# Optimization experiments

Measured on AMD Instinct MI355X. Metric: run time of the kernel, lower is better.

The kernel has to match this reference:

```python
import jax, jax.numpy as jnp
import numpy as np

B, C, T = 32, 1536, 2048
BN = 128  # bottleneck channels


def setup_inputs() -> dict:
    key = jax.random.key(0)
    k1, k2, k3, k4, k5, k6 = jax.random.split(key, 6)
    x = jax.random.normal(k1, (B, C, T), dtype=jnp.float32)
    padding_mask = jax.random.randint(k2, (B, T), 0, 2) == 1
    W_tdnn = jax.random.normal(k3, (BN, C), dtype=jnp.float32) * (1.0 / np.sqrt(C))
    b_tdnn = jax.random.normal(k4, (BN,), dtype=jnp.float32) * 0.01
    W_attn = jax.random.normal(k5, (C, BN), dtype=jnp.float32) * (1.0 / np.sqrt(BN))
    b_attn = jax.random.normal(k6, (C,), dtype=jnp.float32) * 0.01
    return {"x": x, "padding_mask": padding_mask, "W_tdnn": W_tdnn,
            "b_tdnn": b_tdnn, "W_attn": W_attn, "b_attn": b_attn}


def reference(x, padding_mask, W_tdnn, b_tdnn, W_attn, b_attn):
    # pointwise conv1 (k=1) == channel-wise matmul: (B,C,T) -> (B,BN,T)
    e = jnp.tanh(jnp.einsum('oc,bct->bot', W_tdnn, x) + b_tdnn[None, :, None])
    # pointwise conv2: (B,BN,T) -> (B,C,T)
    a = jnp.einsum('co,bot->bct', W_attn, e) + b_attn[None, :, None]
    a = jnp.where(padding_mask[:, None, :], -1e9, a)
    alpha = jax.nn.softmax(a, axis=2)  # (B,C,T)
    mean = jnp.sum(alpha * x, axis=2)  # (B,C)
    var = jnp.sum(alpha * (x - mean[:, :, None]) ** 2, axis=2)
    std = jnp.sqrt(jnp.clip(var, 1e-9, None))
    return jnp.concatenate([mean, std], axis=1)  # (B,2C)
```

## Files before the change

kernel.cpp:

```cpp
#include <hip/hip_runtime.h>
#include <math.h>

#define Bn  32
#define Cn  1536
#define Tn  2048
#define BNn 128
#define SHIFT 12.0f

typedef __attribute__((ext_vector_type(8))) short bf16x8;
typedef __attribute__((ext_vector_type(4))) float fx4;

__device__ __forceinline__ unsigned int f2bf1(float f) {
    unsigned int u = __float_as_uint(f);
    return (u + 0x7fffu + ((u >> 16) & 1u)) >> 16;
}
__device__ __forceinline__ float fast_tanh(float v) {
    return 1.f - 2.f / (__expf(2.f * v) + 1.f);
}

__global__ void k_prep(const float* __restrict__ W1f, const float* __restrict__ Waf,
                       short* __restrict__ W1b, short* __restrict__ Wab) {
    int i = blockIdx.x * 256 + threadIdx.x;
    if (i < BNn * Cn) {
        W1b[i] = (short)f2bf1(W1f[i]);
        Wab[i] = (short)f2bf1(Waf[i]);
    }
}

__global__ __launch_bounds__(256, 3) void k_fused(
    const float* __restrict__ x, const short* __restrict__ W1,
    const float* __restrict__ bias, const short* __restrict__ Wab,
    const int* __restrict__ mask, float* __restrict__ part)
{
    __shared__ short sA[128 * 64];
    __shared__ short sE[128 * 128];

    const int b    = blockIdx.y;
    const int t0g  = blockIdx.x * 128;
    const int tid  = threadIdx.x;
    const int lane = tid & 63;
    const int wv   = tid >> 6;
    const int ln   = lane & 15;
    const int g    = lane >> 4;
    const int wt   = (wv & 1) * 64;
    const int wo   = (wv >> 1) * 64;

    const float* xb = x + (size_t)b * Cn * Tn;
    const float* xt = xb + t0g;

    const int t4 = (tid & 31) * 4;
    const int cq = (tid >> 5) * 4;

    fx4 acc[4][4];
    #pragma unroll
    for (int i = 0; i < 4; ++i)
        #pragma unroll
        for (int j = 0; j < 4; ++j) acc[i][j] = (fx4){0.f, 0.f, 0.f, 0.f};

    for (int k0 = 0; k0 < Cn; k0 += 64) {
        float4 xr[2][4];
        #pragma unroll
        for (int p = 0; p < 2; ++p) {
            const int c = cq + p * 32;
            #pragma unroll
            for (int j = 0; j < 4; ++j)
                xr[p][j] = *(const float4*)(xt + (size_t)(k0 + c + j) * Tn + t4);
        }
        __syncthreads();
        #pragma unroll
        for (int p = 0; p < 2; ++p) {
            const int c   = cq + p * 32;
            const int blk = c >> 3;
            const int sub = c & 7;
            #pragma unroll
            for (int i = 0; i < 4; ++i) {
                const int t = t4 + i;
                unsigned int lo = f2bf1(((const float*)&xr[p][0])[i]) |
                                  (f2bf1(((const float*)&xr[p][1])[i]) << 16);
                unsigned int hi = f2bf1(((const float*)&xr[p][2])[i]) |
                                  (f2bf1(((const float*)&xr[p][3])[i]) << 16);
                const int idx = t * 64 + ((blk ^ (t & 7)) << 3) + sub;
                *(uint2*)(sA + idx) = make_uint2(lo, hi);
            }
        }
        __syncthreads();

        #pragma unroll
        for (int kt = 0; kt < 2; ++kt) {
            bf16x8 bq[4];
            #pragma unroll
            for (int nn = 0; nn < 4; ++nn)
                bq[nn] = *(const bf16x8*)(W1 + (size_t)(wo + nn * 16 + ln) * Cn
                                          + k0 + kt * 32 + g * 8);
            bf16x8 af[4];
            #pragma unroll
            for (int mm = 0; mm < 4; ++mm) {
                const int t = wt + mm * 16 + ln;
                af[mm] = *(const bf16x8*)(sA + t * 64 + (((kt * 4 + g) ^ (t & 7)) << 3));
            }
            #pragma unroll
            for (int mm = 0; mm < 4; ++mm)
                #pragma unroll
                for (int nn = 0; nn < 4; ++nn)
                    acc[mm][nn] = __builtin_amdgcn_mfma_f32_16x16x32_bf16(
                        af[mm], bq[nn], acc[mm][nn], 0, 0, 0);
        }
    }

    float bs[4];
    #pragma unroll
    for (int nn = 0; nn < 4; ++nn) bs[nn] = bias[wo + nn * 16 + ln];

    #pragma unroll
    for (int mm = 0; mm < 4; ++mm)
        #pragma unroll
        for (int nn = 0; nn < 4; ++nn) {
            #pragma unroll
            for (int r = 0; r < 4; ++r) {
                const int t = wt + mm * 16 + g * 4 + r;
                const int o = wo + nn * 16 + ln;
                const float v = fast_tanh(acc[mm][nn][r] + bs[nn]);
                sE[t * 128 + (((o >> 3) ^ (t & 15)) << 3) + (o & 7)] = (short)f2bf1(v);
            }
        }
    __syncthreads();

    bf16x8 af2[4][4];
    #pragma unroll
    for (int mt = 0; mt < 4; ++mt)
        #pragma unroll
        for (int kt = 0; kt < 4; ++kt) {
            const int t = wt + mt * 16 + ln;
            af2[mt][kt] = *(const bf16x8*)(sE + t * 128 + (((kt * 4 + g) ^ (t & 15)) << 3));
        }

    int4 mv[4];
    #pragma unroll
    for (int mt = 0; mt < 4; ++mt)
        mv[mt] = *(const int4*)(mask + (size_t)b * Tn + t0g + wt + mt * 16 + g * 4);

    const int wc    = (wv >> 1) * 32;
    const int chunk = blockIdx.x * 2 + (wv & 1);

    for (int cc = 0; cc < Cn; cc += 64) {
        const int c0 = (Cn - 64) - cc;
        #pragma unroll
        for (int nt = 0; nt < 2; ++nt) {
            const int cr = c0 + wc + nt * 16 + ln;

            bf16x8 bfr[4];
            #pragma unroll
            for (int kt = 0; kt < 4; ++kt)
                bfr[kt] = *(const bf16x8*)(Wab + (size_t)cr * BNn + kt * 32 + g * 8);

            float4 xq[4];
            #pragma unroll
            for (int mt = 0; mt < 4; ++mt)
                xq[mt] = *(const float4*)(xb + (size_t)cr * Tn
                                          + t0g + wt + mt * 16 + g * 4);

            fx4 a2[4];
            #pragma unroll
            for (int mt = 0; mt < 4; ++mt) a2[mt] = (fx4){0.f, 0.f, 0.f, 0.f};

            #pragma unroll
            for (int kt = 0; kt < 4; ++kt)
                #pragma unroll
                for (int mt = 0; mt < 4; ++mt)
                    a2[mt] = __builtin_amdgcn_mfma_f32_16x16x32_bf16(
                        af2[mt][kt], bfr[kt], a2[mt], 0, 0, 0);

            float s0 = 0.f, s1 = 0.f, s2 = 0.f;
            #pragma unroll
            for (int mt = 0; mt < 4; ++mt) {
                #pragma unroll
                for (int r = 0; r < 4; ++r) {
                    const int msk = ((const int*)&mv[mt])[r];
                    const float p = msk ? 0.f : __expf(a2[mt][r] - SHIFT);
                    const float xv = ((const float*)&xq[mt])[r];
                    s0 += p;
                    s1 += p * xv;
                    s2 += p * xv * xv;
                }
            }
            s0 += __shfl_xor(s0, 16); s1 += __shfl_xor(s1, 16); s2 += __shfl_xor(s2, 16);
            s0 += __shfl_xor(s0, 32); s1 += __shfl_xor(s1, 32); s2 += __shfl_xor(s2, 32);
            if (g == 0) {
                *(float4*)&part[(((size_t)b * 32 + chunk) * Cn + cr) * 4] =
                    make_float4(s0, s1, s2, 0.f);
            }
        }
    }
}

__global__ void k_merge(const float* __restrict__ part, float* __restrict__ out) {
    const int i = blockIdx.x * 256 + threadIdx.x;
    if (i >= Bn * Cn) return;
    const int b = i / Cn, c = i - b * Cn;
    float s0 = 0.f, s1 = 0.f, s2 = 0.f;
    #pragma unroll 8
    for (int sp = 0; sp < 32; ++sp) {
        const float4 v = *(const float4*)&part[(((size_t)b * 32 + sp) * Cn + c) * 4];
        s0 += v.x; s1 += v.y; s2 += v.z;
    }
    const float mean = s1 / s0;
    const float var  = fmaxf(s2 / s0 - mean * mean, 1e-9f);
    out[(size_t)b * (2 * Cn) + c]      = mean;
    out[(size_t)b * (2 * Cn) + Cn + c] = sqrtf(var);
}

extern "C" void kernel_launch(void* const* d_in, const int* in_sizes, int n_in,
                              void* d_out, int out_size, void* d_ws, size_t ws_size,
                              hipStream_t stream) {
    const float* x      = (const float*)d_in[0];
    const int*   mask   = (const int*)d_in[1];
    const float* W_tdnn = (const float*)d_in[2];
    const float* b_tdnn = (const float*)d_in[3];
    const float* W_attn = (const float*)d_in[4];
    float* out = (float*)d_out;

    short* W1b  = (short*)d_ws;
    short* Wab  = W1b + (size_t)BNn * Cn;
    float* part = (float*)(Wab + (size_t)BNn * Cn);

    k_prep<<<dim3((BNn * Cn + 255) / 256), 256, 0, stream>>>(W_tdnn, W_attn, W1b, Wab);
    k_fused<<<dim3(Tn / 128, Bn), 256, 0, stream>>>(x, W1b, b_tdnn, Wab, mask, part);
    k_merge<<<dim3((Bn * Cn + 255) / 256), 256, 0, stream>>>(part, out);
}
```

Measured before the change: 632.6 us.

## Software-pipeline global loads in both GEMM phases with register double buffering

Both main loops now use explicit register double buffering. In phase 1, the next 64-channel slice of x is loaded into registers while MFMAs run on the current LDS tile. In phase 2, the next Wab and x fragments are prefetched before the current tile's MFMA, exp and reduction, hiding global load latency behind compute. The extra register buffers raise pressure, so launch bounds drop from 3 to 2 blocks per SM, which lowers occupancy in exchange for intra-wave overlap.

```diff
diff --git a/kernel.cpp b/kernel.cpp
--- a/kernel.cpp
+++ b/kernel.cpp
@@ -27,7 +27,91 @@
     }
 }
 
-__global__ __launch_bounds__(256, 3) void k_fused(
+
+#define P1_LOAD(XR, K0) do {                                                  \
+    _Pragma("unroll") for (int p = 0; p < 2; ++p) {                           \
+        const int c_ = cq + p * 32;                                           \
+        _Pragma("unroll") for (int j = 0; j < 4; ++j)                         \
+            XR[p][j] = *(const float4*)(xt + (size_t)((K0) + c_ + j) * Tn + t4); \
+    }                                                                         \
+} while (0)
+
+#define P1_WRITE(XR) do {                                                     \
+    _Pragma("unroll") for (int p = 0; p < 2; ++p) {                           \
+        const int c_   = cq + p * 32;                                         \
+        const int blk_ = c_ >> 3;                                             \
+        const int sub_ = c_ & 7;                                              \
+        _Pragma("unroll") for (int i2 = 0; i2 < 4; ++i2) {                    \
+            const int t_ = t4 + i2;                                           \
+            unsigned int lo_ = f2bf1(((const float*)&XR[p][0])[i2]) |         \
+                               (f2bf1(((const float*)&XR[p][1])[i2]) << 16);  \
+            unsigned int hi_ = f2bf1(((const float*)&XR[p][2])[i2]) |         \
+                               (f2bf1(((const float*)&XR[p][3])[i2]) << 16);  \
+            const int idx_ = t_ * 64 + ((blk_ ^ (t_ & 7)) << 3) + sub_;       \
+            *(uint2*)(sA + idx_) = make_uint2(lo_, hi_);                      \
+        }                                                                     \
+    }                                                                         \
+} while (0)
+
+#define P1_COMPUTE(K0) do {                                                   \
+    _Pragma("unroll") for (int kt = 0; kt < 2; ++kt) {                        \
+        bf16x8 bq_[4];                                                        \
+        _Pragma("unroll") for (int nn = 0; nn < 4; ++nn)                      \
+            bq_[nn] = *(const bf16x8*)(W1 + (size_t)(wo + nn * 16 + ln) * Cn  \
+                                       + (K0) + kt * 32 + g * 8);             \
+        bf16x8 af_[4];                                                        \
+        _Pragma("unroll") for (int mm = 0; mm < 4; ++mm) {                    \
+            const int t_ = wt + mm * 16 + ln;                                 \
+            af_[mm] = *(const bf16x8*)(sA + t_ * 64                           \
+                                       + (((kt * 4 + g) ^ (t_ & 7)) << 3));   \
+        }                                                                     \
+        _Pragma("unroll") for (int mm = 0; mm < 4; ++mm)                      \
+            _Pragma("unroll") for (int nn = 0; nn < 4; ++nn)                  \
+                acc[mm][nn] = __builtin_amdgcn_mfma_f32_16x16x32_bf16(        \
+                    af_[mm], bq_[nn], acc[mm][nn], 0, 0, 0);                  \
+    }                                                                         \
+} while (0)
+
+#define P2_CR(I) (((Cn - 64) - ((I) >> 1) * 64) + wc + ((I) & 1) * 16 + ln)
+
+#define P2_LOAD(BQ, XQ, I) do {                                               \
+    const int cr_ = P2_CR(I);                                                 \
+    _Pragma("unroll") for (int kt = 0; kt < 4; ++kt)                          \
+        BQ[kt] = *(const bf16x8*)(Wab + (size_t)cr_ * BNn + kt * 32 + g * 8); \
+    _Pragma("unroll") for (int mt = 0; mt < 4; ++mt)                          \
+        XQ[mt] = *(const float4*)(xb + (size_t)cr_ * Tn                       \
+                                  + t0g + wt + mt * 16 + g * 4);              \
+} while (0)
+
+#define P2_COMPUTE(BQ, XQ, I) do {                                           \
+    fx4 a2_[4];                                                               \
+    _Pragma("unroll") for (int mt = 0; mt < 4; ++mt)                          \
+        a2_[mt] = (fx4){0.f, 0.f, 0.f, 0.f};                                  \
+    _Pragma("unroll") for (int kt = 0; kt < 4; ++kt)                          \
+        _Pragma("unroll") for (int mt = 0; mt < 4; ++mt)                      \
+            a2_[mt] = __builtin_amdgcn_mfma_f32_16x16x32_bf16(                \
+                af2[mt][kt], BQ[kt], a2_[mt], 0, 0, 0);                       \
+    float s0_ = 0.f, s1_ = 0.f, s2_ = 0.f;                                    \
+    _Pragma("unroll") for (int mt = 0; mt < 4; ++mt) {                        \
+        _Pragma("unroll") for (int r = 0; r < 4; ++r) {                       \
+            const int msk_ = ((const int*)&mv[mt])[r];                        \
+            const float p_ = msk_ ? 0.f : __expf(a2_[mt][r] - SHIFT);         \
+            const float xv_ = ((const float*)&XQ[mt])[r];                     \
+            s0_ += p_; s1_ += p_ * xv_; s2_ += p_ * xv_ * xv_;                \
+        }                                                                     \
+    }                                                                         \
+    s0_ += __shfl_xor(s0_, 16); s1_ += __shfl_xor(s1_, 16);                   \
+    s2_ += __shfl_xor(s2_, 16);                                               \
+    s0_ += __shfl_xor(s0_, 32); s1_ += __shfl_xor(s1_, 32);                   \
+    s2_ += __shfl_xor(s2_, 32);                                               \
+    if (g == 0) {                                                             \
+        const int cr_ = P2_CR(I);                                             \
+        *(float4*)&part[(((size_t)b * 32 + chunk) * Cn + cr_) * 4] =          \
+            make_float4(s0_, s1_, s2_, 0.f);                                  \
+    }                                                                         \
+} while (0)
+
+__global__ __launch_bounds__(256, 2) void k_fused(
     const float* __restrict__ x, const short* __restrict__ W1,
     const float* __restrict__ bias, const short* __restrict__ Wab,
     const int* __restrict__ mask, float* __restrict__ part)
@@ -57,54 +141,19 @@
         #pragma unroll
         for (int j = 0; j < 4; ++j) acc[i][j] = (fx4){0.f, 0.f, 0.f, 0.f};
 
-    for (int k0 = 0; k0 < Cn; k0 += 64) {
-        float4 xr[2][4];
-        #pragma unroll
-        for (int p = 0; p < 2; ++p) {
-            const int c = cq + p * 32;
-            #pragma unroll
-            for (int j = 0; j < 4; ++j)
-                xr[p][j] = *(const float4*)(xt + (size_t)(k0 + c + j) * Tn + t4);
-        }
-        __syncthreads();
-        #pragma unroll
-        for (int p = 0; p < 2; ++p) {
-            const int c   = cq + p * 32;
-            const int blk = c >> 3;
-            const int sub = c & 7;
-            #pragma unroll
-            for (int i = 0; i < 4; ++i) {
-                const int t = t4 + i;
-                unsigned int lo = f2bf1(((const float*)&xr[p][0])[i]) |
-                                  (f2bf1(((const float*)&xr[p][1])[i]) << 16);
-                unsigned int hi = f2bf1(((const float*)&xr[p][2])[i]) |
-                                  (f2bf1(((const float*)&xr[p][3])[i]) << 16);
-                const int idx = t * 64 + ((blk ^ (t & 7)) << 3) + sub;
-                *(uint2*)(sA + idx) = make_uint2(lo, hi);
-            }
-        }
-        __syncthreads();
-
-        #pragma unroll
-        for (int kt = 0; kt < 2; ++kt) {
-            bf16x8 bq[4];
-            #pragma unroll
-            for (int nn = 0; nn < 4; ++nn)
-                bq[nn] = *(const bf16x8*)(W1 + (size_t)(wo + nn * 16 + ln) * Cn
-                                          + k0 + kt * 32 + g * 8);
-            bf16x8 af[4];
-            #pragma unroll
-            for (int mm = 0; mm < 4; ++mm) {
-                const int t = wt + mm * 16 + ln;
-                af[mm] = *(const bf16x8*)(sA + t * 64 + (((kt * 4 + g) ^ (t & 7)) << 3));
-            }
-            #pragma unroll
-            for (int mm = 0; mm < 4; ++mm)
-                #pragma unroll
-                for (int nn = 0; nn < 4; ++nn)
-                    acc[mm][nn] = __builtin_amdgcn_mfma_f32_16x16x32_bf16(
-                        af[mm], bq[nn], acc[mm][nn], 0, 0, 0);
-        }
+    float4 xrA[2][4], xrB[2][4];
+    P1_LOAD(xrA, 0);
+    for (int k0 = 0; k0 < Cn; k0 += 128) {
+        __syncthreads();
+        P1_WRITE(xrA);
+        __syncthreads();
+        P1_LOAD(xrB, k0 + 64);
+        P1_COMPUTE(k0);
+        __syncthreads();
+        P1_WRITE(xrB);
+        __syncthreads();
+        if (k0 + 128 < Cn) P1_LOAD(xrA, k0 + 128);
+        P1_COMPUTE(k0 + 64);
     }
 
     float bs[4];
@@ -142,54 +191,14 @@
     const int wc    = (wv >> 1) * 32;
     const int chunk = blockIdx.x * 2 + (wv & 1);
 
-    for (int cc = 0; cc < Cn; cc += 64) {
-        const int c0 = (Cn - 64) - cc;
-        #pragma unroll
-        for (int nt = 0; nt < 2; ++nt) {
-            const int cr = c0 + wc + nt * 16 + ln;
-
-            bf16x8 bfr[4];
-            #pragma unroll
-            for (int kt = 0; kt < 4; ++kt)
-                bfr[kt] = *(const bf16x8*)(Wab + (size_t)cr * BNn + kt * 32 + g * 8);
-
-            float4 xq[4];
-            #pragma unroll
-            for (int mt = 0; mt < 4; ++mt)
-                xq[mt] = *(const float4*)(xb + (size_t)cr * Tn
-                                          + t0g + wt + mt * 16 + g * 4);
-
-            fx4 a2[4];
-            #pragma unroll
-            for (int mt = 0; mt < 4; ++mt) a2[mt] = (fx4){0.f, 0.f, 0.f, 0.f};
-
-            #pragma unroll
-            for (int kt = 0; kt < 4; ++kt)
-                #pragma unroll
-                for (int mt = 0; mt < 4; ++mt)
-                    a2[mt] = __builtin_amdgcn_mfma_f32_16x16x32_bf16(
-                        af2[mt][kt], bfr[kt], a2[mt], 0, 0, 0);
-
-            float s0 = 0.f, s1 = 0.f, s2 = 0.f;
-            #pragma unroll
-            for (int mt = 0; mt < 4; ++mt) {
-                #pragma unroll
-                for (int r = 0; r < 4; ++r) {
-                    const int msk = ((const int*)&mv[mt])[r];
-                    const float p = msk ? 0.f : __expf(a2[mt][r] - SHIFT);
-                    const float xv = ((const float*)&xq[mt])[r];
-                    s0 += p;
-                    s1 += p * xv;
-                    s2 += p * xv * xv;
-                }
-            }
-            s0 += __shfl_xor(s0, 16); s1 += __shfl_xor(s1, 16); s2 += __shfl_xor(s2, 16);
-            s0 += __shfl_xor(s0, 32); s1 += __shfl_xor(s1, 32); s2 += __shfl_xor(s2, 32);
-            if (g == 0) {
-                *(float4*)&part[(((size_t)b * 32 + chunk) * Cn + cr) * 4] =
-                    make_float4(s0, s1, s2, 0.f);
-            }
-        }
+    bf16x8 bA[4], bB[4];
+    float4 xA[4], xB[4];
+    P2_LOAD(bA, xA, 0);
+    for (int i = 0; i < 48; i += 2) {
+        P2_LOAD(bB, xB, i + 1);
+        P2_COMPUTE(bA, xA, i);
+        if (i + 2 < 48) P2_LOAD(bA, xA, i + 2);
+        P2_COMPUTE(bB, xB, i + 1);
     }
 }
 
```

Result: no change. 620.8 us (-1.9%).
